# Kernel tuning notes

Hardware: AMD Instinct MI355X
Metric: run time of the kernel (lower is better)

Reference implementation:

```python
import math
import jax, jax.numpy as jnp
import numpy as np

# CoordinateDescentRouter defaults (lucidrains/CoLT5-attention)
N_ITERS, EPS, EPS_INIT, EPS_DECAY, FETCH_K_RATIO = 20, 0.03, 4.0, 0.7, 9.0 / 8.0

B, N, D, G, H, DH, NQ, NKV = 2, 4096, 1024, 2, 16, 64, 1024, 1024
DIM_INNER = H * DH  # 1024


def coor_descent(s, k):
    # s: (b, g, n). Differentiable top-k relaxation via coordinate descent.
    logk = math.log(k)
    eps_sched = [max(EPS_INIT * EPS_DECAY ** i, EPS) for i in range(N_ITERS + 1)]
    b = -s
    a = jnp.zeros_like(s[..., :1])
    for ce in eps_sched[:-1]:
        sb = (s + b) / ce
        a = ce * (logk - jax.scipy.special.logsumexp(sb, axis=-1, keepdims=True))
        b = -jax.nn.relu(s + a)
    return jnp.exp((s + a + b) / eps_sched[-1])


def route(x, routing_tokens, num_tokens):
    # x: (b,n,d), routing_tokens: (g,d) -> indices (b,g,nt), scores (b,g,nt), routed (b,g,nt,d)
    bsz, n, _ = x.shape
    k_cd = min(int(num_tokens * FETCH_K_RATIO), n)
    sim = jnp.einsum('bnd,gd->bgn', x, routing_tokens)
    scores = coor_descent(sim, k_cd)
    scores, idx = jax.lax.top_k(scores, num_tokens)
    # straight-through: forward value 1.0, gradient flows through coor_descent scores
    scores = scores + jax.lax.stop_gradient(1.0 - scores)
    routed = x[jnp.arange(bsz)[:, None, None], idx]
    return idx, scores, routed


def rmsnorm(t, gamma):
    # t: (b,g,n,d); F.normalize over feature dim * sqrt(d) * gamma (g,d)
    norm = jnp.sqrt(jnp.sum(t * t, axis=-1, keepdims=True))
    return t / jnp.maximum(norm, 1e-12) * math.sqrt(t.shape[-1]) * gamma[None, :, None, :]


def grouped_attention(queries, kvs, v_scale, o_scale, gamma_q, gamma_c, wq, wkv, wo, null_kv):
    bsz, g, nq, d = queries.shape
    h, dh = null_kv.shape[2], null_kv.shape[-1]
    qn = rmsnorm(queries, gamma_q)
    cn = rmsnorm(kvs, gamma_c)
    # grouped 1x1 conv == per-group linear; within-group output channel order is (h, dh)
    q = jnp.einsum('bgnd,ged->bgne', qn, wq)
    kv = jnp.einsum('bgnd,ged->bgne', cn, wkv)
    k, v = jnp.split(kv, 2, axis=-1)

    def to_heads(t):
        return t.reshape(bsz, g, t.shape[2], h, dh).transpose(0, 1, 3, 2, 4)  # (b,g,h,n,dh)

    q, k, v = map(to_heads, (q, k, v))
    v = v * v_scale  # (b,g,1,nkv,1) broadcast, applied before null kv concat
    nk = jnp.broadcast_to(null_kv[0][None], (bsz,) + null_kv[0].shape)
    nv = jnp.broadcast_to(null_kv[1][None], (bsz,) + null_kv[1].shape)
    k = jnp.concatenate([nk, k], axis=-2)
    v = jnp.concatenate([nv, v], axis=-2)
    sim = jnp.einsum('bghnd,bghmd->bghnm', q * dh ** -0.5, k)
    attn = jax.nn.softmax(sim, axis=-1)
    o = jnp.einsum('bghnm,bghmd->bghnd', attn, v)
    o = o.transpose(0, 1, 3, 2, 4).reshape(bsz, g, nq, h * dh)
    o = jnp.einsum('bgne,gde->bgnd', o, wo)
    return o * o_scale


def setup_inputs() -> dict:
    key = jax.random.key(0)
    ks = jax.random.split(key, 8)
    inv = 1.0 / math.sqrt(D)
    return {
        'x': jax.random.normal(ks[0], (B, N, D), jnp.float32),
        'rt_q': jax.random.normal(ks[1], (G, D), jnp.float32),
        'rt_kv': jax.random.normal(ks[2], (G, D), jnp.float32),
        'gamma_q': jnp.ones((G, D), jnp.float32),
        'gamma_c': jnp.ones((G, D), jnp.float32),
        'wq': jax.random.normal(ks[3], (G, DIM_INNER, D), jnp.float32) * inv,
        'wkv': jax.random.normal(ks[4], (G, 2 * DIM_INNER, D), jnp.float32) * inv,
        'wo': jax.random.normal(ks[5], (G, D, DIM_INNER), jnp.float32) * inv,
        'null_kv': jax.random.normal(ks[6], (2, G, H, 1, DH), jnp.float32),
        'null_token': jax.random.normal(ks[7], (1, 1, D), jnp.float32),
        'num_routed_queries': NQ,
        'num_routed_key_values': NKV,
    }


def reference(x, rt_q, rt_kv, gamma_q, gamma_c, wq, wkv, wo, null_kv, null_token,
              num_routed_queries, num_routed_key_values):
    bsz, n, d = x.shape
    q_idx, q_scores, queries = route(x, rt_q, num_routed_queries)
    _, kv_scores, key_values = route(x, rt_kv, num_routed_key_values)
    v_scale = kv_scores[:, :, None, :, None]  # (b,g,1,nkv,1)
    o_scale = q_scores[..., None]             # (b,g,nq,1)
    attn_out = grouped_attention(queries, key_values, v_scale, o_scale,
                                 gamma_q, gamma_c, wq, wkv, wo, null_kv)
    # scatter routed outputs back, averaging over experts that picked each token
    flat_idx = q_idx.reshape(bsz, -1)                 # (b, g*nq)
    flat_out = attn_out.reshape(bsz, -1, d)           # (b, g*nq, d)
    bidx = jnp.arange(bsz)[:, None]
    summed = jnp.zeros_like(x).at[bidx, flat_idx].add(flat_out)
    counts = jnp.zeros((bsz, n), x.dtype).at[bidx, flat_idx].add(1.0)
    not_routed = (counts == 0.0)[..., None]
    summed = jnp.where(not_routed, 0.0, summed)
    out = summed / jnp.maximum(counts[..., None], 1e-5)
    out = jnp.where(not_routed, null_token, out)
    return out
```

## Files before the change

kernel.cpp:

```cpp
#include <hip/hip_runtime.h>

typedef __attribute__((ext_vector_type(8))) short short8;
typedef __attribute__((ext_vector_type(4))) short short4v;
typedef __attribute__((ext_vector_type(4))) float f32x4;

#define B_ 2
#define N_ 4096
#define D_ 1024
#define G_ 2
#define H_ 16
#define DH_ 64
#define NSLOT 1088
#define LOGK 7.0492548412558374f
#define ATTN_SCALE 0.18033688011112043f
#define FIXED_M 32.0f

#define BAR() __builtin_amdgcn_s_barrier()
#define WAITV4 asm volatile("s_waitcnt vmcnt(4)" ::: "memory")
#define WAITV0 asm volatile("s_waitcnt vmcnt(0)" ::: "memory")
#define GLDS(src, dst) __builtin_amdgcn_global_load_lds( \
    (const __attribute__((address_space(1))) void*)(src), \
    (__attribute__((address_space(3))) void*)(dst), 16, 0, 0)

__device__ __forceinline__ float bf2f(short s) {
  return __uint_as_float(((unsigned)(unsigned short)s) << 16);
}
__device__ __forceinline__ short f2bf(float f) {
  unsigned u = __float_as_uint(f);
  u = (u + 0x7FFFu + ((u >> 16) & 1u)) >> 16;
  return (short)u;
}
__device__ __forceinline__ short f2bf_trunc(float f) {
  return (short)(__float_as_uint(f) >> 16);
}

__global__ __launch_bounds__(256) void prep_kernel(
    const float* __restrict__ x, const float* __restrict__ rtq,
    const float* __restrict__ rtkv, float* __restrict__ sim,
    const float* __restrict__ null_kv, short* __restrict__ kb_,
    short* __restrict__ vb_)
{
  int bid = blockIdx.x;
  if (bid < 2048) {
    int wid = threadIdx.x >> 6, lane = threadIdx.x & 63;
    int row = bid * 4 + wid;
    int b = row >> 12, n = row & (N_ - 1);
    const float* xr = x + (size_t)row * D_;
    float a0 = 0.f, a1 = 0.f, a2 = 0.f, a3 = 0.f;
#pragma unroll
    for (int c = 0; c < 4; ++c) {
      int d = c * 256 + lane * 4;
      f32x4 xv = *(const f32x4*)(xr + d);
      f32x4 r0 = *(const f32x4*)(rtq + d);
      f32x4 r1 = *(const f32x4*)(rtq + D_ + d);
      f32x4 r2 = *(const f32x4*)(rtkv + d);
      f32x4 r3 = *(const f32x4*)(rtkv + D_ + d);
#pragma unroll
      for (int e = 0; e < 4; ++e) {
        a0 += xv[e] * r0[e];
        a1 += xv[e] * r1[e];
        a2 += xv[e] * r2[e];
        a3 += xv[e] * r3[e];
      }
    }
#pragma unroll
    for (int o = 32; o; o >>= 1) {
      a0 += __shfl_xor(a0, o); a1 += __shfl_xor(a1, o);
      a2 += __shfl_xor(a2, o); a3 += __shfl_xor(a3, o);
    }
    if (lane == 0) {
      sim[((size_t)(b)*G_ + 0) * N_ + n] = a0;
      sim[((size_t)(b)*G_ + 1) * N_ + n] = a1;
      sim[((size_t)(B_ + b)*G_ + 0) * N_ + n] = a2;
      sim[((size_t)(B_ + b)*G_ + 1) * N_ + n] = a3;
    }
  } else {
    int bgh = (bid - 2048) * 4 + (threadIdx.x >> 6);
    int g = (bgh >> 4) & 1, h = bgh & 15;
    int t = threadIdx.x & 63;
    float kvk = null_kv[((size_t)(0 * G_ + g) * H_ + h) * DH_ + t];
    float kvv = null_kv[((size_t)(1 * G_ + g) * H_ + h) * DH_ + t];
    kb_[((size_t)bgh * NSLOT + 1024) * DH_ + t] = f2bf(kvk);
    vb_[((size_t)bgh * DH_ + t) * NSLOT + 1024] = f2bf(kvv);
  }
}

__global__ __launch_bounds__(1024) void topk_wconv(
    const float* __restrict__ sim, int* __restrict__ idxout, int* __restrict__ inv,
    const float* __restrict__ wq, const float* __restrict__ wkv,
    const float* __restrict__ wo, short* __restrict__ dq,
    short* __restrict__ dkv, short* __restrict__ dwo)
{
  if (blockIdx.x >= 8) {
    int base = (blockIdx.x - 8) * 4096 + threadIdx.x;
#pragma unroll
    for (int c = 0; c < 4; ++c) {
      int i = base + c * 1024;
      const float* src; short* dst;
      if (i < 524288) { src = wq; dst = dq; }
      else if (i < 1572864) { src = wkv; dst = dkv; i -= 524288; }
      else { src = wo; dst = dwo; i -= 1572864; }
      f32x4 v = ((const f32x4*)src)[i];
      short4v o;
#pragma unroll
      for (int e = 0; e < 4; ++e) o[e] = f2bf(v[e]);
      ((short4v*)dst)[i] = o;
    }
    return;
  }

  __shared__ float rbm[16];
  __shared__ float rbs[16];
  __shared__ float res;
  __shared__ unsigned keys[N_];
  __shared__ int scanbuf[16];

  int r = blockIdx.x >> 2, b = (blockIdx.x >> 1) & 1, g = blockIdx.x & 1;
  const float* srow = sim + ((size_t)blockIdx.x << 12);
  int tid = threadIdx.x, lane = tid & 63, wid = tid >> 6;

  float sv[4];
#pragma unroll
  for (int j = 0; j < 4; ++j) sv[j] = srow[tid * 4 + j];

  float a = 0.f;
  double epsd = 4.0;
  for (int it = 0; it < 20; ++it) {
    float eps = (float)fmax(epsd, 0.03);
    epsd *= 0.7;
    float sb[4]; float mt = -INFINITY;
#pragma unroll
    for (int j = 0; j < 4; ++j) {
      float bb = (it == 0) ? (-sv[j]) : (-fmaxf(sv[j] + a, 0.f));
      sb[j] = (sv[j] + bb) / eps;
      mt = fmaxf(mt, sb[j]);
    }
#pragma unroll
    for (int o = 32; o; o >>= 1) mt = fmaxf(mt, __shfl_xor(mt, o));
    float st = 0.f;
#pragma unroll
    for (int j = 0; j < 4; ++j) st += expf(sb[j] - mt);
#pragma unroll
    for (int o = 32; o; o >>= 1) st += __shfl_xor(st, o);
    if (lane == 0) { rbm[wid] = mt; rbs[wid] = st; }
    __syncthreads();
    if (tid < 64) {
      float m2 = (tid < 16) ? rbm[tid] : -INFINITY;
      float s2 = (tid < 16) ? rbs[tid] : 0.f;
#pragma unroll
      for (int o = 8; o; o >>= 1) {
        float mo = __shfl_xor(m2, o), so = __shfl_xor(s2, o);
        float mn = fmaxf(m2, mo);
        s2 = s2 * expf(m2 - mn) + so * expf(mo - mn);
        m2 = mn;
      }
      if (tid == 0) res = logf(s2) + m2;
    }
    __syncthreads();
    float lse = res;
    a = eps * (LOGK - lse);
  }
  __syncthreads();

  unsigned kb[4]; int c1 = 0;
#pragma unroll
  for (int j = 0; j < 4; ++j) {
    float sc = expf(fminf(sv[j] + a, 0.f) / 0.03f);
    kb[j] = __float_as_uint(sc);
    keys[tid * 4 + j] = kb[j];
    c1 += (kb[j] == 0x3F800000u);
  }
#pragma unroll
  for (int o = 32; o; o >>= 1) c1 += __shfl_xor(c1, o);
  if (lane == 0) scanbuf[wid] = c1;
  __syncthreads();
  int c1tot = 0;
  for (int i = 0; i < 16; ++i) c1tot += scanbuf[i];
  __syncthreads();

  int flag[4];
  if (c1tot >= 1024) {
#pragma unroll
    for (int j = 0; j < 4; ++j) flag[j] = (kb[j] == 0x3F800000u);
  } else {
#pragma unroll
    for (int j = 0; j < 4; ++j) {
      unsigned kn = kb[j]; int n = tid * 4 + j; int rank = 0;
      for (int m = 0; m < N_; ++m) {
        unsigned km = keys[m];
        rank += (km > kn) || (km == kn && m < n);
      }
      flag[j] = (rank < 1024);
    }
  }

  int cnt = flag[0] + flag[1] + flag[2] + flag[3];
  int inc = cnt;
#pragma unroll
  for (int o = 1; o < 64; o <<= 1) {
    int tt = __shfl_up(inc, o);
    if (lane >= o) inc += tt;
  }
  if (lane == 63) scanbuf[wid] = inc;
  __syncthreads();
  int off = 0;
  for (int w = 0; w < wid; ++w) off += scanbuf[w];
  int pos = off + inc - cnt;
  int* op = idxout + ((size_t)blockIdx.x << 10);
  int* ip = inv + ((size_t)(b * G_ + g) << 12);
#pragma unroll
  for (int j = 0; j < 4; ++j) {
    if (flag[j]) {
      if (pos < 1024) {
        int n = tid * 4 + j;
        op[pos] = n;
        if (r == 0) ip[n] = pos;
      }
      pos++;
    }
  }
}

__global__ __launch_bounds__(256) void gather_rms(
    const float* __restrict__ x, const int* __restrict__ idx,
    const float* __restrict__ gamma_q, const float* __restrict__ gamma_c,
    short* __restrict__ qn, short* __restrict__ cn)
{
  __shared__ float rb[4];
  __shared__ float tot;
  int id = blockIdx.x;
  int r = id >> 12, rem = id & 4095;
  int g = (rem >> 10) & 1;
  int b = rem >> 11;
  int tok = idx[id];
  int t = threadIdx.x;
  const float* xr = x + ((size_t)b * N_ + tok) * D_;
  f32x4 v = *(const f32x4*)(xr + t * 4);
  float ss = v[0]*v[0] + v[1]*v[1] + v[2]*v[2] + v[3]*v[3];
#pragma unroll
  for (int o = 32; o; o >>= 1) ss += __shfl_xor(ss, o);
  if ((t & 63) == 0) rb[t >> 6] = ss;
  __syncthreads();
  if (t == 0) tot = rb[0] + rb[1] + rb[2] + rb[3];
  __syncthreads();
  float scale = 32.0f / fmaxf(sqrtf(tot), 1e-12f);
  const float* gm = (r ? gamma_c : gamma_q) + g * D_;
  f32x4 gv = *(const f32x4*)(gm + t * 4);
  short* dst = (r ? cn : qn) + ((size_t)rem << 10) + t * 4;
  short4v ov;
#pragma unroll
  for (int e = 0; e < 4; ++e) ov[e] = f2bf(v[e] * scale * gv[e]);
  *(short4v*)dst = ov;
}

__global__ __launch_bounds__(256, 3) void gemm_qkv(
    const short* __restrict__ qn, const short* __restrict__ cn,
    const short* __restrict__ wqb, const short* __restrict__ wkvb,
    short* __restrict__ qout, short* __restrict__ kout, short* __restrict__ vout)
{
  __shared__ short As[8192];
  __shared__ short Bs[8192];
  int t = threadIdx.x, lane = t & 63, wid = t >> 6;
  int grp = lane >> 4, l15 = lane & 15;
  int wm = wid >> 1, wn = wid & 1;
  int lin = blockIdx.x + 8 * (blockIdx.y + 24 * blockIdx.z);
  int s = (lin & 7) * 96 + (lin >> 3);
  int bx = s & 7, ny = (s >> 3) % 24, bg = s / 192;
  bool isq = ny < 8;
  const short* A  = isq ? qn : cn;
  const short* Bw = isq ? wqb : wkvb;
  int NB = isq ? 1024 : 2048;
  int nbase = (isq ? ny : ny - 8) * 128;
  float oscale = isq ? ATTN_SCALE : 1.0f;
  int mbase = bx * 128;
  int g = bg & 1;
  const short* Ab = A + ((size_t)bg << 20);
  const short* Bp = Bw + ((size_t)g * NB + nbase) * 1024;

  f32x4 zero = {0.f, 0.f, 0.f, 0.f};
  f32x4 acc[4][4];
#pragma unroll
  for (int i = 0; i < 4; ++i)
#pragma unroll
    for (int j = 0; j < 4; ++j) acc[i][j] = zero;

  const short* apA[4]; const short* apB[4]; int dstoff[4];
#pragma unroll
  for (int c = 0; c < 4; ++c) {
    int u = c * 256 + t;
    int row = u >> 3, j = u & 7;
    int cu = (j ^ (row & 7)) << 3;
    apA[c] = Ab + ((size_t)(mbase + row) << 10) + cu;
    apB[c] = Bp + ((size_t)row << 10) + cu;
    dstoff[c] = c * 2048 + wid * 512;
  }

  for (int kb = 0; kb < 16; ++kb) {
    int ko = kb * 64;
    if (kb) __syncthreads();
#pragma unroll
    for (int c = 0; c < 4; ++c) {
      GLDS(apA[c] + ko, As + dstoff[c]);
      GLDS(apB[c] + ko, Bs + dstoff[c]);
    }
    WAITV0;
    __syncthreads();
    const char* Ac = (const char*)As;
    const char* Bc = (const char*)Bs;
#pragma unroll
    for (int kf = 0; kf < 2; ++kf) {
      short8 af[4], bf_[4];
#pragma unroll
      for (int mt = 0; mt < 4; ++mt) {
        int ra = wm * 64 + mt * 16 + l15;
        af[mt] = *(const short8*)(Ac + ra * 128 + (((grp << 4) + (kf << 6)) ^ ((ra & 7) << 4)));
      }
#pragma unroll
      for (int nt = 0; nt < 4; ++nt) {
        int rb = wn * 64 + nt * 16 + l15;
        bf_[nt] = *(const short8*)(Bc + rb * 128 + (((grp << 4) + (kf << 6)) ^ ((rb & 7) << 4)));
      }
      __builtin_amdgcn_s_setprio(1);
#pragma unroll
      for (int mt = 0; mt < 4; ++mt)
#pragma unroll
        for (int nt = 0; nt < 4; ++nt)
          acc[mt][nt] = __builtin_amdgcn_mfma_f32_16x16x32_bf16(af[mt], bf_[nt], acc[mt][nt], 0, 0, 0);
      __builtin_amdgcn_s_setprio(0);
    }
  }

#pragma unroll
  for (int mt = 0; mt < 4; ++mt)
#pragma unroll
    for (int nt = 0; nt < 4; ++nt) {
      int n = nbase + wn*64 + nt*16 + l15;
#pragma unroll
      for (int rr = 0; rr < 4; ++rr) {
        int m = mbase + wm*64 + mt*16 + grp*4 + rr;
        float v = acc[mt][nt][rr] * oscale;
        if (isq) {
          qout[((size_t)bg * 1024 + m) * 1024 + n] = f2bf(v);
        } else {
          if (n < 1024) {
            kout[(((size_t)bg * H_ + (n >> 6)) * NSLOT + m) * DH_ + (n & 63)] = f2bf(v);
          } else {
            int e = n - 1024;
            vout[(((size_t)bg * H_ + (e >> 6)) * DH_ + (e & 63)) * NSLOT + m] = f2bf(v);
          }
        }
      }
    }
}

__global__ __launch_bounds__(256, 3) void gemm_wo(
    const short* __restrict__ A, const short* __restrict__ Bw,
    short* __restrict__ out0, short* __restrict__ out1)
{
  __shared__ short As[8192];
  __shared__ short Bs[8192];
  int t = threadIdx.x, lane = t & 63, wid = t >> 6;
  int grp = lane >> 4, l15 = lane & 15;
  int wm = wid >> 1, wn = wid & 1;
  int lin = blockIdx.x + 8 * (blockIdx.y + 8 * blockIdx.z);
  int s = (lin & 7) * 64 + (lin >> 3);
  int mbase = (s & 7) * 128, nbase = ((s >> 3) & 7) * 128;
  int z = s >> 6, bg = z >> 1, sp = z & 1, g = bg & 1;
  short* out = sp ? out1 : out0;
  const short* Ab = A + ((size_t)bg << 20);
  const short* Bp = Bw + ((size_t)g * 1024 + nbase) * 1024;

  f32x4 zero = {0.f, 0.f, 0.f, 0.f};
  f32x4 acc[4][4];
#pragma unroll
  for (int i = 0; i < 4; ++i)
#pragma unroll
    for (int j = 0; j < 4; ++j) acc[i][j] = zero;

  const short* apA[4]; const short* apB[4]; int dstoff[4];
#pragma unroll
  for (int c = 0; c < 4; ++c) {
    int u = c * 256 + t;
    int row = u >> 3, j = u & 7;
    int cu = (j ^ (row & 7)) << 3;
    apA[c] = Ab + ((size_t)(mbase + row) << 10) + cu;
    apB[c] = Bp + ((size_t)row << 10) + cu;
    dstoff[c] = c * 2048 + wid * 512;
  }

  int kb0 = sp * 8;
  for (int kk = 0; kk < 8; ++kk) {
    int ko = (kb0 + kk) * 64;
    if (kk) __syncthreads();
#pragma unroll
    for (int c = 0; c < 4; ++c) {
      GLDS(apA[c] + ko, As + dstoff[c]);
      GLDS(apB[c] + ko, Bs + dstoff[c]);
    }
    WAITV0;
    __syncthreads();
    const char* Ac = (const char*)As;
    const char* Bc = (const char*)Bs;
#pragma unroll
    for (int kf = 0; kf < 2; ++kf) {
      short8 af[4], bf_[4];
#pragma unroll
      for (int mt = 0; mt < 4; ++mt) {
        int ra = wm * 64 + mt * 16 + l15;
        af[mt] = *(const short8*)(Ac + ra * 128 + (((grp << 4) + (kf << 6)) ^ ((ra & 7) << 4)));
      }
#pragma unroll
      for (int nt = 0; nt < 4; ++nt) {
        int rb = wn * 64 + nt * 16 + l15;
        bf_[nt] = *(const short8*)(Bc + rb * 128 + (((grp << 4) + (kf << 6)) ^ ((rb & 7) << 4)));
      }
      __builtin_amdgcn_s_setprio(1);
#pragma unroll
      for (int mt = 0; mt < 4; ++mt)
#pragma unroll
        for (int nt = 0; nt < 4; ++nt)
          acc[mt][nt] = __builtin_amdgcn_mfma_f32_16x16x32_bf16(af[mt], bf_[nt], acc[mt][nt], 0, 0, 0);
      __builtin_amdgcn_s_setprio(0);
    }
  }

#pragma unroll
  for (int mt = 0; mt < 4; ++mt)
#pragma unroll
    for (int nt = 0; nt < 4; ++nt) {
      int n = nbase + wn*64 + nt*16 + l15;
#pragma unroll
      for (int rr = 0; rr < 4; ++rr) {
        int m = mbase + wm*64 + mt*16 + grp*4 + rr;
        out[((size_t)bg * 1024 + m) * 1024 + n] = f2bf(acc[mt][nt][rr]);
      }
    }
}

__global__ __launch_bounds__(256, 3) void attn_kernel(
    const short* __restrict__ q, const short* __restrict__ k,
    const short* __restrict__ vT, short* __restrict__ o0)
{
  __shared__ short Ks[2][4096];
  __shared__ short Vs[2][4096];
  __shared__ short Ps[4][32 * 72];
  int bgh = blockIdx.x, qb = blockIdx.y;
  int bg = bgh >> 4, h = bgh & 15;
  int wid = threadIdx.x >> 6, lane = threadIdx.x & 63;
  int l15 = lane & 15, grp = lane >> 4;
  int qbase = qb * 128 + wid * 32;
  short* Pw = &Ps[wid][0];

  short8 bq[2][2];
#pragma unroll
  for (int qh = 0; qh < 2; ++qh) {
    const short* qp = q + ((size_t)bg * 1024 + qbase + qh * 16 + l15) * 1024 + h * 64 + (grp << 3);
    bq[qh][0] = *(const short8*)qp;
    bq[qh][1] = *(const short8*)(qp + 32);
  }
  short8 ones8;
  short ov = (l15 == 0) ? (short)0x3F80 : (short)0;
#pragma unroll
  for (int e = 0; e < 8; ++e) ones8[e] = ov;

  int u0 = wid * 128 + lane, u1 = u0 + 64;
  int r0 = u0 >> 3, j0 = u0 & 7, r1 = u1 >> 3, j1 = u1 & 7;
  const short* kbase = k + (size_t)bgh * NSLOT * DH_;
  const short* vbase = vT + (size_t)bgh * DH_ * NSLOT;
  const short* kss0 = kbase + r0 * 64 + ((j0 ^ (r0 & 7)) << 3);
  const short* kss1 = kbase + r1 * 64 + ((j1 ^ (r1 & 7)) << 3);
  const short* vss0 = vbase + (size_t)r0 * NSLOT + ((j0 ^ (r0 & 7)) << 3);
  const short* vss1 = vbase + (size_t)r1 * NSLOT + ((j1 ^ (r1 & 7)) << 3);

  f32x4 zero = {0.f, 0.f, 0.f, 0.f};
  f32x4 minit = {-FIXED_M, -FIXED_M, -FIXED_M, -FIXED_M};
  f32x4 oacc[2][4], lacc[2];
#pragma unroll
  for (int qh = 0; qh < 2; ++qh) {
    lacc[qh] = zero;
#pragma unroll
    for (int dt = 0; dt < 4; ++dt) oacc[qh][dt] = zero;
  }

  auto STAGE = [&](int tile, int p) {
    size_t ko = (size_t)tile * 4096;
    size_t vo = (size_t)tile * 64;
    short* kd = &Ks[p][0] + wid * 1024;
    short* vd = &Vs[p][0] + wid * 1024;
    GLDS(kss0 + ko, kd);
    GLDS(kss1 + ko, kd + 512);
    GLDS(vss0 + vo, vd);
    GLDS(vss1 + vo, vd + 512);
  };

  auto PROCESS = [&](int tile, int p) {
    const char* Kc = (const char*)&Ks[p][0];
    const char* Vc = (const char*)&Vs[p][0];
    f32x4 sacc[2][4];
#pragma unroll
    for (int qh = 0; qh < 2; ++qh)
#pragma unroll
      for (int kt = 0; kt < 4; ++kt) sacc[qh][kt] = minit;
#pragma unroll
    for (int kf = 0; kf < 2; ++kf) {
      short8 ka[4];
#pragma unroll
      for (int kt = 0; kt < 4; ++kt) {
        int ra = kt * 16 + l15;
        ka[kt] = *(const short8*)(Kc + ra * 128 + (((grp + 4 * kf) ^ (ra & 7)) << 4));
      }
      __builtin_amdgcn_s_setprio(1);
#pragma unroll
      for (int kt = 0; kt < 4; ++kt)
#pragma unroll
        for (int qh = 0; qh < 2; ++qh)
          sacc[qh][kt] = __builtin_amdgcn_mfma_f32_16x16x32_bf16(ka[kt], bq[qh][kf], sacc[qh][kt], 0, 0, 0);
      __builtin_amdgcn_s_setprio(0);
    }
    if (tile == 16) {
#pragma unroll
      for (int qh = 0; qh < 2; ++qh)
#pragma unroll
        for (int kt = 0; kt < 4; ++kt)
#pragma unroll
          for (int rr = 0; rr < 4; ++rr)
            if ((kt * 16 + (grp << 2) + rr) != 0) sacc[qh][kt][rr] = -INFINITY;
    }
#pragma unroll
    for (int qh = 0; qh < 2; ++qh)
#pragma unroll
      for (int kt = 0; kt < 4; ++kt) {
        short4v pk;
#pragma unroll
        for (int rr = 0; rr < 4; ++rr) pk[rr] = f2bf_trunc(exp2f(sacc[qh][kt][rr]));
        *(short4v*)(Pw + (qh * 16 + l15) * 72 + kt * 16 + (grp << 2)) = pk;
      }
#pragma unroll
    for (int ks = 0; ks < 2; ++ks) {
      short8 pa[2];
#pragma unroll
      for (int qh = 0; qh < 2; ++qh)
        pa[qh] = *(const short8*)((const char*)Pw + (qh * 16 + l15) * 144 + grp * 16 + ks * 64);
      __builtin_amdgcn_s_setprio(1);
#pragma unroll
      for (int dt = 0; dt < 4; ++dt) {
        int ra = dt * 16 + l15;
        short8 vbf = *(const short8*)(Vc + ra * 128 + (((grp + 4 * ks) ^ (ra & 7)) << 4));
#pragma unroll
        for (int qh = 0; qh < 2; ++qh)
          oacc[qh][dt] = __builtin_amdgcn_mfma_f32_16x16x32_bf16(pa[qh], vbf, oacc[qh][dt], 0, 0, 0);
      }
#pragma unroll
      for (int qh = 0; qh < 2; ++qh)
        lacc[qh] = __builtin_amdgcn_mfma_f32_16x16x32_bf16(pa[qh], ones8, lacc[qh], 0, 0, 0);
      __builtin_amdgcn_s_setprio(0);
    }
  };

  STAGE(0, 0);
  STAGE(1, 1);
  WAITV4;
  BAR();
  for (int tile = 0; tile < 17; ++tile) {
    int p = tile & 1;
    PROCESS(tile, p);
    if (tile + 1 < 17) {
      BAR();
      if (tile + 2 < 17) { STAGE(tile + 2, p); WAITV4; }
      else               { WAITV0; }
      BAR();
    }
  }

#pragma unroll
  for (int qh = 0; qh < 2; ++qh)
#pragma unroll
    for (int rr = 0; rr < 4; ++rr) {
      float lv = __shfl(lacc[qh][rr], grp << 4);
      float inv_l = 1.0f / lv;
      int qq = qh * 16 + (grp << 2) + rr;
#pragma unroll
      for (int dt = 0; dt < 4; ++dt) {
        int dh = dt * 16 + l15;
        o0[((size_t)bg * 1024 + qbase + qq) * 1024 + h * 64 + dh] =
            f2bf(oacc[qh][dt][rr] * inv_l);
      }
    }
}

__global__ __launch_bounds__(256) void finalize_kernel(
    const short* __restrict__ wo0, const short* __restrict__ wo1,
    const int* __restrict__ inv, const float* __restrict__ null_token,
    float* __restrict__ outp)
{
  int id = blockIdx.x;
  int b = id >> 12, n = id & (N_ - 1);
  int s0 = inv[((size_t)(b * G_ + 0) << 12) + n];
  int s1 = inv[((size_t)(b * G_ + 1) << 12) + n];
  int t = threadIdx.x;
  float* dst = outp + (size_t)id * D_ + t * 4;
  if (s0 < 0 && s1 < 0) {
    *(f32x4*)dst = *(const f32x4*)(null_token + t * 4);
  } else {
    f32x4 sum = {0.f, 0.f, 0.f, 0.f};
    float cnt = 0.f;
    if (s0 >= 0) {
      size_t loc = (((size_t)(b * G_ + 0) * 1024 + s0) << 10) + t * 4;
      short4v v = *(const short4v*)(wo0 + loc);
      short4v v2 = *(const short4v*)(wo1 + loc);
#pragma unroll
      for (int e = 0; e < 4; ++e) sum[e] += bf2f(v[e]) + bf2f(v2[e]);
      cnt += 1.f;
    }
    if (s1 >= 0) {
      size_t loc = (((size_t)(b * G_ + 1) * 1024 + s1) << 10) + t * 4;
      short4v v = *(const short4v*)(wo0 + loc);
      short4v v2 = *(const short4v*)(wo1 + loc);
#pragma unroll
      for (int e = 0; e < 4; ++e) sum[e] += bf2f(v[e]) + bf2f(v2[e]);
      cnt += 1.f;
    }
    f32x4 rv;
#pragma unroll
    for (int e = 0; e < 4; ++e) rv[e] = sum[e] / cnt;
    *(f32x4*)dst = rv;
  }
}

extern "C" void kernel_launch(void* const* d_in, const int* in_sizes, int n_in,
                              void* d_out, int out_size, void* d_ws, size_t ws_size,
                              hipStream_t stream) {
  (void)in_sizes; (void)n_in; (void)out_size; (void)ws_size;
  const float* x        = (const float*)d_in[0];
  const float* rt_q     = (const float*)d_in[1];
  const float* rt_kv    = (const float*)d_in[2];
  const float* gamma_q  = (const float*)d_in[3];
  const float* gamma_c  = (const float*)d_in[4];
  const float* wq       = (const float*)d_in[5];
  const float* wkv      = (const float*)d_in[6];
  const float* wo       = (const float*)d_in[7];
  const float* null_kv  = (const float*)d_in[8];
  const float* null_tok = (const float*)d_in[9];
  float* outp = (float*)d_out;

  char* ws = (char*)d_ws;
  size_t off = 0;
  auto alloc = [&](size_t bytes) { char* p = ws + off; off += (bytes + 255) & ~(size_t)255; return p; };
  float* sim   = (float*)alloc((size_t)2 * B_ * G_ * N_ * 4);
  int*   idx   = (int*)  alloc((size_t)2 * B_ * G_ * 1024 * 4);
  int*   inv   = (int*)  alloc((size_t)B_ * G_ * N_ * 4);
  short* qn    = (short*)alloc((size_t)B_ * G_ * 1024 * 1024 * 2);
  short* cn    = (short*)alloc((size_t)B_ * G_ * 1024 * 1024 * 2);
  short* qproj = (short*)alloc((size_t)B_ * G_ * 1024 * 1024 * 2);
  size_t kvbytes = (size_t)B_ * G_ * H_ * NSLOT * DH_ * 2;
  short* kbuf  = (short*)alloc(kvbytes);
  short* vbuf  = (short*)alloc(kvbytes);
  short* obuf  = (short*)alloc((size_t)B_ * G_ * 1024 * 1024 * 2);
  short* wobuf = (short*)alloc((size_t)B_ * G_ * 1024 * 1024 * 2);
  short* wo_bf = (short*)alloc((size_t)G_ * 1024 * 1024 * 2);
  short* wq_bf  = wobuf;
  short* wkv_bf = obuf;
  short* wobuf2 = qproj;

  hipMemsetAsync(inv, 0xFF, (size_t)B_ * G_ * N_ * 4, stream);

  prep_kernel<<<2064, 256, 0, stream>>>(x, rt_q, rt_kv, sim, null_kv, kbuf, vbuf);
  topk_wconv<<<520, 1024, 0, stream>>>(sim, idx, inv, wq, wkv, wo,
                                       wq_bf, wkv_bf, wo_bf);
  gather_rms<<<2 * B_ * G_ * 1024, 256, 0, stream>>>(x, idx, gamma_q, gamma_c, qn, cn);
  gemm_qkv<<<dim3(8, 24, B_ * G_), 256, 0, stream>>>(qn, cn, wq_bf, wkv_bf, qproj, kbuf, vbuf);
  attn_kernel<<<dim3(64, 8), 256, 0, stream>>>(qproj, kbuf, vbuf, obuf);
  gemm_wo<<<dim3(8, 8, 2 * B_ * G_), 256, 0, stream>>>(obuf, wo_bf, wobuf, wobuf2);
  finalize_kernel<<<B_ * N_, 256, 0, stream>>>(wobuf, wobuf2, inv, null_tok, outp);
}
```

Measured before the change: 158.2 us.

## Overlap next K-tile global-to-LDS load with MFMA in QKV and Wo GEMMs

Restructures the single-buffered GEMM main loops so each iteration reads the second half of the current LDS tile, then the first half into registers, synchronizes, and starts the async global-to-LDS load of the next tile before issuing the remaining MFMAs. This hides part of the load latency behind compute instead of serializing load, wait and compute. It also moves the null-kv initialization from prep_kernel into extra blocks of topk_wconv. The reordered k-half accumulation changes summation order slightly, and the extra barriers add sync cost.

Result: no change. 157.0 us (-0.8%).

```diff
diff --git a/kernel.cpp b/kernel.cpp
--- a/kernel.cpp
+++ b/kernel.cpp
@@ -18,6 +18,8 @@
 #define BAR() __builtin_amdgcn_s_barrier()
 #define WAITV4 asm volatile("s_waitcnt vmcnt(4)" ::: "memory")
 #define WAITV0 asm volatile("s_waitcnt vmcnt(0)" ::: "memory")
+#define LGKM0() do { asm volatile("s_waitcnt lgkmcnt(0)" ::: "memory"); \
+                     __builtin_amdgcn_sched_barrier(0); } while (0)
 #define GLDS(src, dst) __builtin_amdgcn_global_load_lds( \
     (const __attribute__((address_space(1))) void*)(src), \
     (__attribute__((address_space(3))) void*)(dst), 16, 0, 0)
@@ -36,61 +38,60 @@
 
 __global__ __launch_bounds__(256) void prep_kernel(
     const float* __restrict__ x, const float* __restrict__ rtq,
-    const float* __restrict__ rtkv, float* __restrict__ sim,
+    const float* __restrict__ rtkv, float* __restrict__ sim)
+{
+  int wid = threadIdx.x >> 6, lane = threadIdx.x & 63;
+  int row = blockIdx.x * 4 + wid;
+  int b = row >> 12, n = row & (N_ - 1);
+  const float* xr = x + (size_t)row * D_;
+  float a0 = 0.f, a1 = 0.f, a2 = 0.f, a3 = 0.f;
+#pragma unroll
+  for (int c = 0; c < 4; ++c) {
+    int d = c * 256 + lane * 4;
+    f32x4 xv = *(const f32x4*)(xr + d);
+    f32x4 r0 = *(const f32x4*)(rtq + d);
+    f32x4 r1 = *(const f32x4*)(rtq + D_ + d);
+    f32x4 r2 = *(const f32x4*)(rtkv + d);
+    f32x4 r3 = *(const f32x4*)(rtkv + D_ + d);
+#pragma unroll
+    for (int e = 0; e < 4; ++e) {
+      a0 += xv[e] * r0[e];
+      a1 += xv[e] * r1[e];
+      a2 += xv[e] * r2[e];
+      a3 += xv[e] * r3[e];
+    }
+  }
+#pragma unroll
+  for (int o = 32; o; o >>= 1) {
+    a0 += __shfl_xor(a0, o); a1 += __shfl_xor(a1, o);
+    a2 += __shfl_xor(a2, o); a3 += __shfl_xor(a3, o);
+  }
+  if (lane == 0) {
+    sim[((size_t)(b)*G_ + 0) * N_ + n] = a0;
+    sim[((size_t)(b)*G_ + 1) * N_ + n] = a1;
+    sim[((size_t)(B_ + b)*G_ + 0) * N_ + n] = a2;
+    sim[((size_t)(B_ + b)*G_ + 1) * N_ + n] = a3;
+  }
+}
+
+__global__ __launch_bounds__(1024) void topk_wconv(
+    const float* __restrict__ sim, int* __restrict__ idxout, int* __restrict__ inv,
+    const float* __restrict__ wq, const float* __restrict__ wkv,
+    const float* __restrict__ wo, short* __restrict__ dq,
+    short* __restrict__ dkv, short* __restrict__ dwo,
     const float* __restrict__ null_kv, short* __restrict__ kb_,
     short* __restrict__ vb_)
 {
-  int bid = blockIdx.x;
-  if (bid < 2048) {
-    int wid = threadIdx.x >> 6, lane = threadIdx.x & 63;
-    int row = bid * 4 + wid;
-    int b = row >> 12, n = row & (N_ - 1);
-    const float* xr = x + (size_t)row * D_;
-    float a0 = 0.f, a1 = 0.f, a2 = 0.f, a3 = 0.f;
-#pragma unroll
-    for (int c = 0; c < 4; ++c) {
-      int d = c * 256 + lane * 4;
-      f32x4 xv = *(const f32x4*)(xr + d);
-      f32x4 r0 = *(const f32x4*)(rtq + d);
-      f32x4 r1 = *(const f32x4*)(rtq + D_ + d);
-      f32x4 r2 = *(const f32x4*)(rtkv + d);
-      f32x4 r3 = *(const f32x4*)(rtkv + D_ + d);
-#pragma unroll
-      for (int e = 0; e < 4; ++e) {
-        a0 += xv[e] * r0[e];
-        a1 += xv[e] * r1[e];
-        a2 += xv[e] * r2[e];
-        a3 += xv[e] * r3[e];
-      }
-    }
-#pragma unroll
-    for (int o = 32; o; o >>= 1) {
-      a0 += __shfl_xor(a0, o); a1 += __shfl_xor(a1, o);
-      a2 += __shfl_xor(a2, o); a3 += __shfl_xor(a3, o);
-    }
-    if (lane == 0) {
-      sim[((size_t)(b)*G_ + 0) * N_ + n] = a0;
-      sim[((size_t)(b)*G_ + 1) * N_ + n] = a1;
-      sim[((size_t)(B_ + b)*G_ + 0) * N_ + n] = a2;
-      sim[((size_t)(B_ + b)*G_ + 1) * N_ + n] = a3;
-    }
-  } else {
-    int bgh = (bid - 2048) * 4 + (threadIdx.x >> 6);
+  if (blockIdx.x >= 520) {
+    int bgh = (blockIdx.x - 520) * 16 + (threadIdx.x >> 6);
     int g = (bgh >> 4) & 1, h = bgh & 15;
     int t = threadIdx.x & 63;
     float kvk = null_kv[((size_t)(0 * G_ + g) * H_ + h) * DH_ + t];
     float kvv = null_kv[((size_t)(1 * G_ + g) * H_ + h) * DH_ + t];
     kb_[((size_t)bgh * NSLOT + 1024) * DH_ + t] = f2bf(kvk);
     vb_[((size_t)bgh * DH_ + t) * NSLOT + 1024] = f2bf(kvv);
-  }
-}
-
-__global__ __launch_bounds__(1024) void topk_wconv(
-    const float* __restrict__ sim, int* __restrict__ idxout, int* __restrict__ inv,
-    const float* __restrict__ wq, const float* __restrict__ wkv,
-    const float* __restrict__ wo, short* __restrict__ dq,
-    short* __restrict__ dkv, short* __restrict__ dwo)
-{
+    return;
+  }
   if (blockIdx.x >= 8) {
     int base = (blockIdx.x - 8) * 4096 + threadIdx.x;
 #pragma unroll
@@ -295,38 +296,63 @@
     dstoff[c] = c * 2048 + wid * 512;
   }
 
-  for (int kb = 0; kb < 16; ++kb) {
+  auto STAGE = [&](int kb) {
     int ko = kb * 64;
-    if (kb) __syncthreads();
 #pragma unroll
     for (int c = 0; c < 4; ++c) {
       GLDS(apA[c] + ko, As + dstoff[c]);
       GLDS(apB[c] + ko, Bs + dstoff[c]);
     }
-    WAITV0;
-    __syncthreads();
-    const char* Ac = (const char*)As;
-    const char* Bc = (const char*)Bs;
-#pragma unroll
-    for (int kf = 0; kf < 2; ++kf) {
-      short8 af[4], bf_[4];
-#pragma unroll
-      for (int mt = 0; mt < 4; ++mt) {
-        int ra = wm * 64 + mt * 16 + l15;
-        af[mt] = *(const short8*)(Ac + ra * 128 + (((grp << 4) + (kf << 6)) ^ ((ra & 7) << 4)));
-      }
-#pragma unroll
-      for (int nt = 0; nt < 4; ++nt) {
-        int rb = wn * 64 + nt * 16 + l15;
-        bf_[nt] = *(const short8*)(Bc + rb * 128 + (((grp << 4) + (kf << 6)) ^ ((rb & 7) << 4)));
-      }
-      __builtin_amdgcn_s_setprio(1);
-#pragma unroll
-      for (int mt = 0; mt < 4; ++mt)
-#pragma unroll
-        for (int nt = 0; nt < 4; ++nt)
-          acc[mt][nt] = __builtin_amdgcn_mfma_f32_16x16x32_bf16(af[mt], bf_[nt], acc[mt][nt], 0, 0, 0);
-      __builtin_amdgcn_s_setprio(0);
+  };
+
+  STAGE(0);
+  WAITV0;
+  BAR();
+
+  const char* Ac = (const char*)As;
+  const char* Bc = (const char*)Bs;
+  for (int kb = 0; kb < 16; ++kb) {
+    short8 af1[4], bf1[4], af0[4], bf0[4];
+#pragma unroll
+    for (int mt = 0; mt < 4; ++mt) {
+      int ra = wm * 64 + mt * 16 + l15;
+      af1[mt] = *(const short8*)(Ac + ra * 128 + ((16 + 64) << 0 ? (((grp << 4) + 64) ^ ((ra & 7) << 4)) : 0));
+    }
+#pragma unroll
+    for (int nt = 0; nt < 4; ++nt) {
+      int rb = wn * 64 + nt * 16 + l15;
+      bf1[nt] = *(const short8*)(Bc + rb * 128 + (((grp << 4) + 64) ^ ((rb & 7) << 4)));
+    }
+    __builtin_amdgcn_s_setprio(1);
+#pragma unroll
+    for (int mt = 0; mt < 4; ++mt)
+#pragma unroll
+      for (int nt = 0; nt < 4; ++nt)
+        acc[mt][nt] = __builtin_amdgcn_mfma_f32_16x16x32_bf16(af1[mt], bf1[nt], acc[mt][nt], 0, 0, 0);
+    __builtin_amdgcn_s_setprio(0);
+#pragma unroll
+    for (int mt = 0; mt < 4; ++mt) {
+      int ra = wm * 64 + mt * 16 + l15;
+      af0[mt] = *(const short8*)(Ac + ra * 128 + (((grp << 4)) ^ ((ra & 7) << 4)));
+    }
+#pragma unroll
+    for (int nt = 0; nt < 4; ++nt) {
+      int rb = wn * 64 + nt * 16 + l15;
+      bf0[nt] = *(const short8*)(Bc + rb * 128 + (((grp << 4)) ^ ((rb & 7) << 4)));
+    }
+    LGKM0();
+    BAR();
+    if (kb + 1 < 16) STAGE(kb + 1);
+    __builtin_amdgcn_s_setprio(1);
+#pragma unroll
+    for (int mt = 0; mt < 4; ++mt)
+#pragma unroll
+      for (int nt = 0; nt < 4; ++nt)
+        acc[mt][nt] = __builtin_amdgcn_mfma_f32_16x16x32_bf16(af0[mt], bf0[nt], acc[mt][nt], 0, 0, 0);
+    __builtin_amdgcn_s_setprio(0);
+    if (kb + 1 < 16) {
+      WAITV0;
+      BAR();
     }
   }
 
@@ -388,39 +414,64 @@
     dstoff[c] = c * 2048 + wid * 512;
   }
 
-  int kb0 = sp * 8;
-  for (int kk = 0; kk < 8; ++kk) {
-    int ko = (kb0 + kk) * 64;
-    if (kk) __syncthreads();
+  auto STAGE = [&](int kb) {
+    int ko = kb * 64;
 #pragma unroll
     for (int c = 0; c < 4; ++c) {
       GLDS(apA[c] + ko, As + dstoff[c]);
       GLDS(apB[c] + ko, Bs + dstoff[c]);
     }
-    WAITV0;
-    __syncthreads();
-    const char* Ac = (const char*)As;
-    const char* Bc = (const char*)Bs;
-#pragma unroll
-    for (int kf = 0; kf < 2; ++kf) {
-      short8 af[4], bf_[4];
-#pragma unroll
-      for (int mt = 0; mt < 4; ++mt) {
-        int ra = wm * 64 + mt * 16 + l15;
-        af[mt] = *(const short8*)(Ac + ra * 128 + (((grp << 4) + (kf << 6)) ^ ((ra & 7) << 4)));
-      }
-#pragma unroll
-      for (int nt = 0; nt < 4; ++nt) {
-        int rb = wn * 64 + nt * 16 + l15;
-        bf_[nt] = *(const short8*)(Bc + rb * 128 + (((grp << 4) + (kf << 6)) ^ ((rb & 7) << 4)));
-      }
-      __builtin_amdgcn_s_setprio(1);
-#pragma unroll
-      for (int mt = 0; mt < 4; ++mt)
-#pragma unroll
-        for (int nt = 0; nt < 4; ++nt)
-          acc[mt][nt] = __builtin_amdgcn_mfma_f32_16x16x32_bf16(af[mt], bf_[nt], acc[mt][nt], 0, 0, 0);
-      __builtin_amdgcn_s_setprio(0);
+  };
+
+  int kb0 = sp * 8;
+  STAGE(kb0);
+  WAITV0;
+  BAR();
+
+  const char* Ac = (const char*)As;
+  const char* Bc = (const char*)Bs;
+  for (int kk = 0; kk < 8; ++kk) {
+    short8 af1[4], bf1[4], af0[4], bf0[4];
+#pragma unroll
+    for (int mt = 0; mt < 4; ++mt) {
+      int ra = wm * 64 + mt * 16 + l15;
+      af1[mt] = *(const short8*)(Ac + ra * 128 + (((grp << 4) + 64) ^ ((ra & 7) << 4)));
+    }
+#pragma unroll
+    for (int nt = 0; nt < 4; ++nt) {
+      int rb = wn * 64 + nt * 16 + l15;
+      bf1[nt] = *(const short8*)(Bc + rb * 128 + (((grp << 4) + 64) ^ ((rb & 7) << 4)));
+    }
+    __builtin_amdgcn_s_setprio(1);
+#pragma unroll
+    for (int mt = 0; mt < 4; ++mt)
+#pragma unroll
+      for (int nt = 0; nt < 4; ++nt)
+        acc[mt][nt] = __builtin_amdgcn_mfma_f32_16x16x32_bf16(af1[mt], bf1[nt], acc[mt][nt], 0, 0, 0);
+    __builtin_amdgcn_s_setprio(0);
+#pragma unroll
+    for (int mt = 0; mt < 4; ++mt) {
+      int ra = wm * 64 + mt * 16 + l15;
+      af0[mt] = *(const short8*)(Ac + ra * 128 + (((grp << 4)) ^ ((ra & 7) << 4)));
+    }
+#pragma unroll
+    for (int nt = 0; nt < 4; ++nt) {
+      int rb = wn * 64 + nt * 16 + l15;
+      bf0[nt] = *(const short8*)(Bc + rb * 128 + (((grp << 4)) ^ ((rb & 7) << 4)));
+    }
+    LGKM0();
+    BAR();
+    if (kk + 1 < 8) STAGE(kb0 + kk + 1);
+    __builtin_amdgcn_s_setprio(1);
+#pragma unroll
+    for (int mt = 0; mt < 4; ++mt)
+#pragma unroll
+      for (int nt = 0; nt < 4; ++nt)
+        acc[mt][nt] = __builtin_amdgcn_mfma_f32_16x16x32_bf16(af0[mt], bf0[nt], acc[mt][nt], 0, 0, 0);
+    __builtin_amdgcn_s_setprio(0);
+    if (kk + 1 < 8) {
+      WAITV0;
+      BAR();
     }
   }
 
@@ -664,9 +715,10 @@
 
   hipMemsetAsync(inv, 0xFF, (size_t)B_ * G_ * N_ * 4, stream);
 
-  prep_kernel<<<2064, 256, 0, stream>>>(x, rt_q, rt_kv, sim, null_kv, kbuf, vbuf);
-  topk_wconv<<<520, 1024, 0, stream>>>(sim, idx, inv, wq, wkv, wo,
-                                       wq_bf, wkv_bf, wo_bf);
+  prep_kernel<<<2048, 256, 0, stream>>>(x, rt_q, rt_kv, sim);
+  topk_wconv<<<524, 1024, 0, stream>>>(sim, idx, inv, wq, wkv, wo,
+                                       wq_bf, wkv_bf, wo_bf,
+                                       null_kv, kbuf, vbuf);
   gather_rms<<<2 * B_ * G_ * 1024, 256, 0, stream>>>(x, idx, gamma_q, gamma_c, qn, cn);
   gemm_qkv<<<dim3(8, 24, B_ * G_), 256, 0, stream>>>(qn, cn, wq_bf, wkv_bf, qproj, kbuf, vbuf);
   attn_kernel<<<dim3(64, 8), 256, 0, stream>>>(qproj, kbuf, vbuf, obuf);
```
